# Kernel optimization log

Measured on AMD Instinct MI355X. Metric: run time of the kernel, lower is better.

Reference implementation:

```python
import jax, jax.numpy as jnp
import numpy as np

K = 1.0          # manifold curvature parameter (Lorentz hyperboloid <x,x>_L = -K)
NUM_HEADS = 16
LN_EPS = 1e-5
MID_EPS = 1e-8


def add_time(space):
    # lift a space-like vector onto the hyperboloid: x0 = sqrt(||s||^2 + K)
    t = jnp.sqrt(jnp.sum(space * space, axis=-1, keepdims=True) + K)
    return jnp.concatenate([t, space], axis=-1)


def hlinear(x, W, b):
    # Lorentz linear: dense map on full ambient vector -> space part, recompute time
    return add_time(jnp.einsum('...d,od->...o', x, W) + b)


def hyp_layernorm(x, g, b):
    s = x[..., 1:]
    mu = jnp.mean(s, axis=-1, keepdims=True)
    var = jnp.mean((s - mu) ** 2, axis=-1, keepdims=True)
    s = (s - mu) * jax.lax.rsqrt(var + LN_EPS) * g + b
    return add_time(s)


def hyp_relu(x):
    return add_time(jax.nn.relu(x[..., 1:]))


def lorentz_norm(v):
    # sqrt(|<v,v>_L|) with clamp for numerical safety
    inner = -v[..., 0] ** 2 + jnp.sum(v[..., 1:] ** 2, axis=-1)
    return jnp.sqrt(jnp.maximum(jnp.abs(inner), MID_EPS))


def midpoint_pair(z, x):
    # manifold.midpoint(stack([z, x], dim=-2)).squeeze(): mean then project back
    ave = 0.5 * (z + x)
    return jnp.sqrt(K) * ave / lorentz_norm(ave)[..., None]


def attention(x, Wq, bq, Wk, bk, Wv, bv, Wo, bo):
    B, S, D = x.shape
    dim = D - 1
    H = NUM_HEADS
    dh = dim // H

    def split_heads(t):
        # drop time, split space into heads, re-lift each head onto hyperboloid
        s = t[..., 1:].reshape(B, S, H, dh).transpose(0, 2, 1, 3)  # [B,H,S,dh]
        return add_time(s)                                          # [B,H,S,dh+1]

    qh = split_heads(hlinear(x, Wq, bq))
    kh = split_heads(hlinear(x, Wk, bk))
    vh = split_heads(hlinear(x, Wv, bv))

    # pairwise Lorentz inner product; scores = -d_L^2 / sqrt(dh)
    inner = (jnp.einsum('bhid,bhjd->bhij', qh[..., 1:], kh[..., 1:])
             - qh[..., 0][..., :, None] * kh[..., 0][..., None, :])
    scores = (2.0 / K + 2.0 * inner) / jnp.sqrt(jnp.asarray(dh, x.dtype))
    att = jax.nn.softmax(scores, axis=-1)

    # Lorentz midpoint aggregation of values (weights sum to 1)
    ave = jnp.einsum('bhij,bhjd->bhid', att, vh)
    out = jnp.sqrt(K) * ave / lorentz_norm(ave)[..., None]  # [B,H,S,dh+1]

    # concat head space parts, re-lift, output projection
    out_space = out[..., 1:].transpose(0, 2, 1, 3).reshape(B, S, dim)
    return hlinear(add_time(out_space), Wo, bo)


def reference(x, Wq, bq, Wk, bk, Wv, bv, Wo, bo, ln1_g, ln1_b, W1, c1, W2, c2, ln2_g, ln2_b):
    z = attention(x, Wq, bq, Wk, bk, Wv, bv, Wo, bo)
    x = midpoint_pair(z, x)
    x = hyp_layernorm(x, ln1_g, ln1_b)
    h = hyp_relu(hlinear(x, W1, c1))
    z = hlinear(h, W2, c2)
    x = midpoint_pair(z, x)
    x = hyp_layernorm(x, ln2_g, ln2_b)
    return x


def setup_inputs() -> dict:
    key = jax.random.key(0)
    ks = jax.random.split(key, 12)
    B, S, dim, mlp = 4, 1024, 1024, 4096
    D = dim + 1
    sc = 0.02
    x = add_time(jax.random.normal(ks[0], (B, S, dim), dtype=jnp.float32))
    return {
        'x': x,
        'Wq': sc * jax.random.normal(ks[1], (dim, D), dtype=jnp.float32),
        'bq': jnp.zeros((dim,), jnp.float32),
        'Wk': sc * jax.random.normal(ks[2], (dim, D), dtype=jnp.float32),
        'bk': jnp.zeros((dim,), jnp.float32),
        'Wv': sc * jax.random.normal(ks[3], (dim, D), dtype=jnp.float32),
        'bv': jnp.zeros((dim,), jnp.float32),
        'Wo': sc * jax.random.normal(ks[4], (dim, D), dtype=jnp.float32),
        'bo': jnp.zeros((dim,), jnp.float32),
        'ln1_g': jnp.ones((dim,), jnp.float32),
        'ln1_b': jnp.zeros((dim,), jnp.float32),
        'W1': sc * jax.random.normal(ks[5], (mlp, D), dtype=jnp.float32),
        'c1': jnp.zeros((mlp,), jnp.float32),
        'W2': sc * jax.random.normal(ks[6], (dim, mlp + 1), dtype=jnp.float32),
        'c2': jnp.zeros((dim,), jnp.float32),
        'ln2_g': jnp.ones((dim,), jnp.float32),
        'ln2_b': jnp.zeros((dim,), jnp.float32),
    }
```

## Files before the change

### kernel.cpp

```cpp
#include <hip/hip_runtime.h>

typedef unsigned short u16;
typedef unsigned int   u32;
typedef short bf16x8 __attribute__((ext_vector_type(8)));
typedef float f32x4  __attribute__((ext_vector_type(4)));

#define NTOK 4096
#define SEQ  1024

__device__ __forceinline__ u16 f2bf(float f){
  union { float f; u32 u; } x; x.f = f;
  u32 r = (x.u + 0x7FFFu + ((x.u >> 16) & 1u)) >> 16;
  return (u16)r;
}
__device__ __forceinline__ float bf2f(u16 u){
  union { u32 u; float f; } x; x.u = ((u32)u) << 16; return x.f;
}
__device__ __forceinline__ void gl_lds16(const void* gp, void* lp){
  __builtin_amdgcn_global_load_lds(
      (const __attribute__((address_space(1))) u32*)gp,
      (__attribute__((address_space(3))) u32*)lp, 16, 0, 0);
}

__global__ __launch_bounds__(256) void conv_x(const float* __restrict__ x,
                                              u16* __restrict__ xs, float* __restrict__ xt){
  int t = blockIdx.x * 256 + threadIdx.x;
  int tok = t >> 10, i = t & 1023;
  xs[t] = f2bf(x[(size_t)tok * 1025 + 1 + i]);
  if (i == 0) xt[tok] = x[(size_t)tok * 1025];
}

__global__ __launch_bounds__(256) void conv_w_all(
    const float* __restrict__ Wq, const float* __restrict__ Wk,
    const float* __restrict__ Wv, const float* __restrict__ Wo,
    const float* __restrict__ W1, const float* __restrict__ W2,
    u16* __restrict__ wqkv, u16* __restrict__ wo_s, u16* __restrict__ w1_s, u16* __restrict__ w2_s,
    float* __restrict__ wqkv0, float* __restrict__ wo0, float* __restrict__ w10, float* __restrict__ w20)
{
  int t = blockIdx.x * 256 + threadIdx.x;
  const int M1 = 1 << 20;
  const float* W; u16* Wb; float* w0; int shift; int idx;
  if (t < 4 * M1){
    int region = t >> 20; idx = t & (M1 - 1); shift = 10;
    if (region == 0)      { W = Wq; Wb = wqkv;          w0 = wqkv0; }
    else if (region == 1) { W = Wk; Wb = wqkv + M1;     w0 = wqkv0 + 1024; }
    else if (region == 2) { W = Wv; Wb = wqkv + 2 * M1; w0 = wqkv0 + 2048; }
    else                  { W = Wo; Wb = wo_s;          w0 = wo0; }
  } else if (t < 8 * M1){
    idx = t - 4 * M1; shift = 10; W = W1; Wb = w1_s; w0 = w10;
  } else {
    idx = t - 8 * M1; shift = 12; W = W2; Wb = w2_s; w0 = w20;
  }
  int Kin = 1 << shift;
  int r = idx >> shift, i = idx & (Kin - 1);
  Wb[idx] = f2bf(W[(size_t)r * (Kin + 1) + 1 + i]);
  if (i == 0) w0[r] = W[(size_t)r * (Kin + 1)];
}

__global__ __launch_bounds__(256) void v_transpose(const u16* __restrict__ qkv,
                                                   const float* __restrict__ vtm,
                                                   u16* __restrict__ vT){
  __shared__ u16 tile[64 * 72];
  const int tid = threadIdx.x;
  const int kt = blockIdx.x, bh = blockIdx.y;
  const int b = bh >> 4, h = bh & 15;
  #pragma unroll
  for (int i = 0; i < 2; i++){
    int c = tid * 2 + i;
    int key = c >> 3, fc = c & 7;
    uint4 v = *(const uint4*)(qkv + ((size_t)(b * 1024 + kt * 64 + key)) * 3072 + 2048 + h * 64 + fc * 8);
    *(uint4*)&tile[key * 72 + fc * 8] = v;
  }
  __syncthreads();
  for (int c = tid; c < 520; c += 256){
    int vtr = c >> 3, kc = c & 7;
    union { uint4 v; u16 s[8]; } d;
    if (vtr == 0){
      #pragma unroll
      for (int j = 0; j < 8; j++) d.s[j] = f2bf(vtm[(size_t)bh * 1024 + kt * 64 + kc * 8 + j]);
    } else {
      int f = vtr - 1;
      #pragma unroll
      for (int j = 0; j < 8; j++) d.s[j] = tile[(kc * 8 + j) * 72 + f];
    }
    *(uint4*)(vT + ((size_t)bh * 65 + vtr) * 1024 + kt * 64 + kc * 8) = d.v;
  }
}

__global__ __launch_bounds__(256) void gemm_bt(
    const u16* __restrict__ A, int lda, const u16* __restrict__ Bm, int ldb,
    const float* __restrict__ at, int at_mode, const float* __restrict__ b0,
    const float* __restrict__ bias_a, const float* __restrict__ bias_b, const float* __restrict__ bias_c,
    u16* __restrict__ Cbf, int ldc, int Kslice, int mode,
    float* __restrict__ qtv, float* __restrict__ ktv, float* __restrict__ vtm,
    float* __restrict__ rowsq)
{
  __shared__ u16 As[2][128 * 32];
  __shared__ u16 Bs[2][128 * 32];
  const int tid = threadIdx.x;
  const int w = tid >> 6, l = tid & 63;
  const int l15 = l & 15, q = l >> 4;
  const int m0 = blockIdx.y * 128, n0 = blockIdx.x * 128;
  const int ks = blockIdx.z;
  const int kbeg = ks * Kslice;
  const int kend = kbeg + Kslice;
  const int wr = w >> 1, wc = w & 1;
  f32x4 acc[4][4] = {};

  auto stage = [&](int kt, int buf){
    #pragma unroll
    for (int i = 0; i < 2; i++){
      int s = (w * 2 + i) * 64 + l;
      int row = s >> 2;
      int kc = ((s & 3) - (s >> 3)) & 3;
      gl_lds16(A  + (size_t)(m0 + row) * lda + kt + kc * 8,
               &As[buf][(w * 2 + i) * 512]);
      gl_lds16(Bm + (size_t)(n0 + row) * ldb + kt + kc * 8,
               &Bs[buf][(w * 2 + i) * 512]);
    }
  };
  auto compute = [&](int buf){
    bf16x8 af[4], bfr[4];
    #pragma unroll
    for (int i = 0; i < 4; i++){
      int row = wr * 64 + i * 16 + l15;
      int slot = row * 4 + ((q + (row >> 1)) & 3);
      af[i] = *(const bf16x8*)&As[buf][slot * 8];
    }
    #pragma unroll
    for (int j = 0; j < 4; j++){
      int row = wc * 64 + j * 16 + l15;
      int slot = row * 4 + ((q + (row >> 1)) & 3);
      bfr[j] = *(const bf16x8*)&Bs[buf][slot * 8];
    }
    #pragma unroll
    for (int i = 0; i < 4; i++)
      #pragma unroll
      for (int j = 0; j < 4; j++)
        acc[i][j] = __builtin_amdgcn_mfma_f32_16x16x32_bf16(af[i], bfr[j], acc[i][j], 0, 0, 0);
  };

  stage(kbeg, 0);
  for (int kt = kbeg; kt < kend; kt += 64){
    __syncthreads();
    stage(kt + 32, 1);
    compute(0);
    __syncthreads();
    if (kt + 64 < kend) stage(kt + 64, 0);
    compute(1);
  }

  const size_t slice_off = (size_t)ks * (size_t)(gridDim.y * 128) * ldc;
  #pragma unroll
  for (int i = 0; i < 4; i++){
    float atv[4];
    #pragma unroll
    for (int r = 0; r < 4; r++){
      float a = at[m0 + wr * 64 + i * 16 + q * 4 + r];
      atv[r] = at_mode ? sqrtf(a + 1.f) : a;
    }
    float p[4] = {0.f, 0.f, 0.f, 0.f};
    #pragma unroll
    for (int j = 0; j < 4; j++){
      int col = n0 + wc * 64 + j * 16 + l15;
      float b0v = b0[col];
      float bv;
      if (mode == 0) bv = (col < 1024) ? bias_a[col] : (col < 2048) ? bias_b[col - 1024] : bias_c[col - 2048];
      else bv = bias_a[col];
      #pragma unroll
      for (int r = 0; r < 4; r++){
        size_t row = (size_t)(m0 + wr * 64 + i * 16 + q * 4 + r);
        float add = (ks == 0) ? (atv[r] * b0v + bv) : 0.f;
        float v = acc[i][j][r] + add;
        if (mode == 2) v = fmaxf(v, 0.f);
        Cbf[slice_off + row * ldc + col] = f2bf(v);
        if (mode != 1) p[r] += v * v;
      }
    }
    if (mode != 1){
      #pragma unroll
      for (int r = 0; r < 4; r++){
        float s = p[r];
        s += __shfl_xor(s, 1, 64); s += __shfl_xor(s, 2, 64);
        s += __shfl_xor(s, 4, 64); s += __shfl_xor(s, 8, 64);
        if (l15 == 0){
          int row = m0 + wr * 64 + i * 16 + q * 4 + r;
          if (mode == 2){
            atomicAdd(&rowsq[row], s);
          } else {
            int ch = (n0 + wc * 64) >> 6;
            int bb = row >> 10, sidx = row & 1023;
            float t = sqrtf(s + 1.f);
            if (ch < 16)      qtv[((size_t)bb * 16 + ch) * 1024 + sidx] = t;
            else if (ch < 32) ktv[((size_t)bb * 16 + ch - 16) * 1024 + sidx] = t;
            else              vtm[((size_t)bb * 16 + ch - 32) * 1024 + sidx] = t;
          }
        }
      }
    }
  }
}

__global__ __launch_bounds__(512) void attn_kernel(
    const u16* __restrict__ qkv, const float* __restrict__ qt,
    const float* __restrict__ ktm, const u16* __restrict__ vT,
    u16* __restrict__ aout, float* __restrict__ aot_sq)
{
  __shared__ u16 smem[30720];
  u16* Qlds = smem;
  u16* Kl0 = smem + 8192;
  u16* Kl1 = smem + 12288;
  u16* Vl0 = smem + 16384;
  u16* Vl1 = smem;
  u16* Plds = smem + 21504;
  const int tid = threadIdx.x;
  const int w = tid >> 6, l = tid & 63;
  const int l15 = l & 15, qd = l >> 4;
  const int q0 = blockIdx.x * 128;
  const int bh = blockIdx.y;
  const int b = bh >> 4, h = bh & 15;
  const size_t tokbase = (size_t)b << 10;

  #pragma unroll
  for (int i = 0; i < 2; i++){
    int c = i * 512 + w * 64 + l;
    int row = c >> 3, kc = ((c & 7) - row) & 7;
    gl_lds16(qkv + (tokbase + q0 + row) * 3072 + h * 64 + kc * 8, &Qlds[(i * 512 + w * 64) * 8]);
  }
  __syncthreads();
  bf16x8 aq[2];
  {
    int row = w * 16 + l15;
    #pragma unroll
    for (int kk = 0; kk < 2; kk++)
      aq[kk] = *(const bf16x8*)&Qlds[(row * 8 + ((kk * 4 + qd + row) & 7)) * 8];
  }
  float tq[4];
  #pragma unroll
  for (int r = 0; r < 4; r++)
    tq[r] = qt[(size_t)bh * SEQ + q0 + w * 16 + qd * 4 + r];

  auto stage_kv = [&](int kt, int buf){
    u16* K = buf ? Kl1 : Kl0;
    u16* V = buf ? Vl1 : Vl0;
    int c = w * 64 + l;
    int row = c >> 3, kc = ((c & 7) - row) & 7;
    gl_lds16(qkv + (tokbase + kt * 64 + row) * 3072 + 1024 + h * 64 + kc * 8, &K[w * 512]);
    gl_lds16(vT + ((size_t)bh * 65 + row) * 1024 + kt * 64 + kc * 8, &V[w * 512]);
    if (w == 0 && l < 8)
      gl_lds16(vT + ((size_t)bh * 65 + 64) * 1024 + kt * 64 + (l & 7) * 8, &V[4096]);
  };

  float mrow[4] = {-1e30f, -1e30f, -1e30f, -1e30f};
  f32x4 acco[5] = {};

  stage_kv(0, 0);
  for (int kt = 0; kt < 16; kt++){
    __syncthreads();
    if (kt + 1 < 16) stage_kv(kt + 1, (kt + 1) & 1);
    u16* K = (kt & 1) ? Kl1 : Kl0;
    u16* V = (kt & 1) ? Vl1 : Vl0;

    float sc[4][4];
    float mx[4] = {-1e30f, -1e30f, -1e30f, -1e30f};
    #pragma unroll
    for (int ct = 0; ct < 4; ct++){
      f32x4 z = {0.f, 0.f, 0.f, 0.f};
      int key = ct * 16 + l15;
      #pragma unroll
      for (int kk = 0; kk < 2; kk++){
        bf16x8 bk = *(const bf16x8*)&K[(key * 8 + ((kk * 4 + qd + key) & 7)) * 8];
        z = __builtin_amdgcn_mfma_f32_16x16x32_bf16(aq[kk], bk, z, 0, 0, 0);
      }
      float tk = ktm[(size_t)bh * SEQ + kt * 64 + key];
      #pragma unroll
      for (int r = 0; r < 4; r++){
        float s = 0.25f + 0.25f * (z[r] - tq[r] * tk);
        sc[ct][r] = s;
        mx[r] = fmaxf(mx[r], s);
      }
    }
    #pragma unroll
    for (int r = 0; r < 4; r++){
      #pragma unroll
      for (int msk = 1; msk < 16; msk <<= 1)
        mx[r] = fmaxf(mx[r], __shfl_xor(mx[r], msk, 64));
      float mnew = fmaxf(mrow[r], mx[r]);
      float alpha = __expf(mrow[r] - mnew);
      mrow[r] = mnew;
      #pragma unroll
      for (int co = 0; co < 5; co++) acco[co][r] *= alpha;
      mx[r] = mnew;
    }
    #pragma unroll
    for (int ct = 0; ct < 4; ct++)
      #pragma unroll
      for (int r = 0; r < 4; r++)
        Plds[w * 1152 + (qd * 4 + r) * 72 + ct * 16 + l15] = f2bf(__expf(sc[ct][r] - mx[r]));
    asm volatile("s_waitcnt lgkmcnt(0)" ::: "memory");
    bf16x8 ap[2];
    #pragma unroll
    for (int kk = 0; kk < 2; kk++)
      ap[kk] = *(const bf16x8*)&Plds[w * 1152 + l15 * 72 + kk * 32 + qd * 8];
    #pragma unroll
    for (int co = 0; co < 5; co++){
      int vtr = co * 16 + l15;
      #pragma unroll
      for (int kk = 0; kk < 2; kk++){
        bf16x8 bv = *(const bf16x8*)&V[(vtr * 8 + ((kk * 4 + qd + vtr) & 7)) * 8];
        acco[co] = __builtin_amdgcn_mfma_f32_16x16x32_bf16(ap[kk], bv, acco[co], 0, 0, 0);
      }
    }
  }
  #pragma unroll
  for (int r = 0; r < 4; r++){
    float ss = 0.f;
    #pragma unroll
    for (int co = 0; co < 5; co++){
      int col = co * 16 + l15;
      float v = acco[co][r];
      if (col == 0) ss -= v * v;
      else if (col < 65) ss += v * v;
    }
    #pragma unroll
    for (int msk = 1; msk < 16; msk <<= 1) ss += __shfl_xor(ss, msk, 64);
    float v0b = __shfl(acco[0][r], l & 48, 64);
    float sp = ss + v0b * v0b;
    float rn = rsqrtf(fmaxf(fabsf(ss), 1e-8f));
    size_t rowg = tokbase + q0 + w * 16 + qd * 4 + r;
    if (l15 == 0) atomicAdd(&aot_sq[rowg], sp * rn * rn);
    #pragma unroll
    for (int co = 0; co < 5; co++){
      int col = co * 16 + l15;
      if (col >= 1 && col < 65)
        aout[rowg * 1024 + h * 64 + col - 1] = f2bf(acco[co][r] * rn);
    }
  }
}

__device__ __forceinline__ float block_sum(float v, float* red){
  int tid = threadIdx.x;
  #pragma unroll
  for (int m = 1; m < 64; m <<= 1) v += __shfl_xor(v, m, 64);
  __syncthreads();
  if ((tid & 63) == 0) red[tid >> 6] = v;
  __syncthreads();
  return red[0] + red[1] + red[2] + red[3];
}

__global__ __launch_bounds__(256) void mid_ln(
    const u16* __restrict__ z, const u16* __restrict__ xsb, const float* __restrict__ xtv,
    const float* __restrict__ gam, const float* __restrict__ bet,
    u16* __restrict__ ob, float* __restrict__ ot,
    float* __restrict__ ofull, int mode_out, int nsl)
{
  __shared__ float red[4];
  const int tid = threadIdx.x;
  const int tok = blockIdx.x;
  float zv[4], xv[4], xtime;
  xtime = xtv[tok];
  {
    const u16* xr = xsb + (size_t)tok * 1024;
    #pragma unroll
    for (int j = 0; j < 4; j++) xv[j] = bf2f(xr[tid + j * 256]);
  }
  {
    #pragma unroll
    for (int j = 0; j < 4; j++) zv[j] = 0.f;
    for (int s = 0; s < nsl; s++){
      const u16* zs = z + (size_t)s * NTOK * 1024 + (size_t)tok * 1024;
      #pragma unroll
      for (int j = 0; j < 4; j++) zv[j] += bf2f(zs[tid + j * 256]);
    }
  }
  float ssz = 0.f;
  #pragma unroll
  for (int j = 0; j < 4; j++) ssz += zv[j] * zv[j];
  ssz = block_sum(ssz, red);
  float tz = sqrtf(ssz + 1.f);
  float av[4]; float ssa = 0.f;
  #pragma unroll
  for (int j = 0; j < 4; j++){ av[j] = 0.5f * (zv[j] + xv[j]); ssa += av[j] * av[j]; }
  ssa = block_sum(ssa, red);
  float avt = 0.5f * (tz + xtime);
  float rn = rsqrtf(fmaxf(fabsf(ssa - avt * avt), 1e-8f));
  float uv[4]; float su = 0.f, squ = 0.f;
  #pragma unroll
  for (int j = 0; j < 4; j++){ uv[j] = av[j] * rn; su += uv[j]; squ += uv[j] * uv[j]; }
  su = block_sum(su, red);
  squ = block_sum(squ, red);
  float mu = su * (1.f / 1024.f);
  float var = squ * (1.f / 1024.f) - mu * mu;
  float rv = rsqrtf(fmaxf(var, 0.f) + 1e-5f);
  float sv[4]; float sss = 0.f;
  #pragma unroll
  for (int j = 0; j < 4; j++){
    int i = tid + j * 256;
    sv[j] = (uv[j] - mu) * rv * gam[i] + bet[i];
    sss += sv[j] * sv[j];
  }
  sss = block_sum(sss, red);
  float tout = sqrtf(sss + 1.f);
  if (mode_out == 0){
    #pragma unroll
    for (int j = 0; j < 4; j++){
      int i = tid + j * 256;
      ob[(size_t)tok * 1024 + i] = f2bf(sv[j]);
    }
    if (tid == 0) ot[tok] = tout;
  } else {
    float* orow = ofull + (size_t)tok * 1025;
    #pragma unroll
    for (int j = 0; j < 4; j++) orow[1 + tid + j * 256] = sv[j];
    if (tid == 0) orow[0] = tout;
  }
}

extern "C" void kernel_launch(void* const* d_in, const int* in_sizes, int n_in,
                              void* d_out, int out_size, void* d_ws, size_t ws_size,
                              hipStream_t stream){
  const float* x   = (const float*)d_in[0];
  const float* Wq  = (const float*)d_in[1];
  const float* bq  = (const float*)d_in[2];
  const float* Wk  = (const float*)d_in[3];
  const float* bk  = (const float*)d_in[4];
  const float* Wv  = (const float*)d_in[5];
  const float* bv  = (const float*)d_in[6];
  const float* Wo  = (const float*)d_in[7];
  const float* bo  = (const float*)d_in[8];
  const float* g1  = (const float*)d_in[9];
  const float* be1 = (const float*)d_in[10];
  const float* W1  = (const float*)d_in[11];
  const float* c1  = (const float*)d_in[12];
  const float* W2  = (const float*)d_in[13];
  const float* c2  = (const float*)d_in[14];
  const float* g2  = (const float*)d_in[15];
  const float* be2 = (const float*)d_in[16];
  float* out = (float*)d_out;

  char* p = (char*)d_ws;
  auto take = [&](size_t n){ char* r = p; p += (n + 255) & ~(size_t)255; return r; };
  u16*   xs    = (u16*)  take((size_t)NTOK * 1024 * 2);
  float* xt    = (float*)take(NTOK * 4);
  u16*   wqkv  = (u16*)  take((size_t)3072 * 1024 * 2);
  float* wqkv0 = (float*)take(3072 * 4);
  u16*   wo_s  = (u16*)  take((size_t)1024 * 1024 * 2);
  float* wo0   = (float*)take(1024 * 4);
  u16*   w1_s  = (u16*)  take((size_t)4096 * 1024 * 2);
  float* w10   = (float*)take(4096 * 4);
  u16*   w2_s  = (u16*)  take((size_t)1024 * 4096 * 2);
  float* w20   = (float*)take(1024 * 4);
  u16*   qkvb  = (u16*)  take((size_t)NTOK * 3072 * 2);
  float* qtv   = (float*)take((size_t)64 * 1024 * 4);
  float* ktv   = (float*)take((size_t)64 * 1024 * 4);
  float* vtm   = (float*)take((size_t)64 * 1024 * 4);
  u16*   vT    = (u16*)  take((size_t)64 * 65 * 1024 * 2);
  u16*   aoutb = (u16*)  take((size_t)NTOK * 1024 * 2);
  float* sqbuf = (float*)take((size_t)2 * NTOK * 4);
  float* aot_sq = sqbuf;
  float* htv_sq = sqbuf + NTOK;
  u16*   zbuf  = (u16*)  take((size_t)4 * NTOK * 1024 * 2);
  u16*   x1b   = (u16*)  take((size_t)NTOK * 1024 * 2);
  float* x1t   = (float*)take(NTOK * 4);
  u16*   hbuf  = (u16*)  take((size_t)NTOK * 4096 * 2);

  hipMemsetAsync(sqbuf, 0, (size_t)2 * NTOK * 4, stream);

  conv_x<<<NTOK * 1024 / 256, 256, 0, stream>>>(x, xs, xt);
  conv_w_all<<<(12 * 1024 * 1024) / 256, 256, 0, stream>>>(
      Wq, Wk, Wv, Wo, W1, W2, wqkv, wo_s, w1_s, w2_s, wqkv0, wo0, w10, w20);

  gemm_bt<<<dim3(24, 32), 256, 0, stream>>>(xs, 1024, wqkv, 1024, xt, 0, wqkv0,
      bq, bk, bv, qkvb, 3072, 1024, 0, qtv, ktv, vtm, nullptr);
  v_transpose<<<dim3(16, 64), 256, 0, stream>>>(qkvb, vtm, vT);
  attn_kernel<<<dim3(8, 64), 512, 0, stream>>>(qkvb, qtv, ktv, vT, aoutb, aot_sq);
  gemm_bt<<<dim3(8, 32, 2), 256, 0, stream>>>(aoutb, 1024, wo_s, 1024, aot_sq, 1, wo0,
      bo, nullptr, nullptr, zbuf, 1024, 512, 1, nullptr, nullptr, nullptr, nullptr);
  mid_ln<<<NTOK, 256, 0, stream>>>(zbuf, xs, xt, g1, be1,
      x1b, x1t, nullptr, 0, 2);
  gemm_bt<<<dim3(32, 32), 256, 0, stream>>>(x1b, 1024, w1_s, 1024, x1t, 0, w10,
      c1, nullptr, nullptr, hbuf, 4096, 1024, 2, nullptr, nullptr, nullptr, htv_sq);
  gemm_bt<<<dim3(8, 32, 4), 256, 0, stream>>>(hbuf, 4096, w2_s, 4096, htv_sq, 1, w20,
      c2, nullptr, nullptr, zbuf, 1024, 1024, 1, nullptr, nullptr, nullptr, nullptr);
  mid_ln<<<NTOK, 256, 0, stream>>>(zbuf, x1b, x1t, g2, be2,
      nullptr, nullptr, out, 1, 4);
}
```

Measured before the change: 467.9 us.

## Rewrite GEMM main loop with register-staged prefetch, tile swizzle, and deeper split-K

Replaces the direct global-to-LDS loads in gemm_bt with global loads into registers that are written to LDS one step later, giving a two-deep prefetch pipeline. Raw s_barrier and waitcnt instructions are issued between sched_barrier fences, and MFMA issue priority is raised. Workgroups are swizzled so that neighbouring blocks share input tiles in cache. The output projection moves from 2-way to 4-way split-K, with the matching mid_ln reduction count updated. This adds register pressure, and the hand-placed barriers could hurt if the compiler's own scheduling was already better.

Result: slower. 728.3 us (+55.7%).

```diff
diff --git a/kernel.cpp b/kernel.cpp
--- a/kernel.cpp
+++ b/kernel.cpp
@@ -7,6 +7,8 @@
 
 #define NTOK 4096
 #define SEQ  1024
+
+#define SCHEDW() __builtin_amdgcn_sched_barrier(0)
 
 __device__ __forceinline__ u16 f2bf(float f){
   union { float f; u32 u; } x; x.f = f;
@@ -88,69 +90,92 @@
 }
 
 __global__ __launch_bounds__(256) void gemm_bt(
-    const u16* __restrict__ A, int lda, const u16* __restrict__ Bm, int ldb,
+    const u16* __restrict__ Ag, int lda, const u16* __restrict__ Bg, int ldb,
     const float* __restrict__ at, int at_mode, const float* __restrict__ b0,
     const float* __restrict__ bias_a, const float* __restrict__ bias_b, const float* __restrict__ bias_c,
     u16* __restrict__ Cbf, int ldc, int Kslice, int mode,
     float* __restrict__ qtv, float* __restrict__ ktv, float* __restrict__ vtm,
     float* __restrict__ rowsq)
 {
-  __shared__ u16 As[2][128 * 32];
-  __shared__ u16 Bs[2][128 * 32];
+  __shared__ u16 A0[4096], A1[4096], B0[4096], B1[4096];
   const int tid = threadIdx.x;
   const int w = tid >> 6, l = tid & 63;
   const int l15 = l & 15, q = l >> 4;
-  const int m0 = blockIdx.y * 128, n0 = blockIdx.x * 128;
+  const int wr = w >> 1, wc = w & 1;
+  const int gx = gridDim.x;
+  const int nwg = gx * gridDim.y;
+  const int lin = blockIdx.y * gx + blockIdx.x;
+  const int swz = (lin & 7) * (nwg >> 3) + (lin >> 3);
+  const int m0 = (swz / gx) * 128, n0 = (swz % gx) * 128;
   const int ks = blockIdx.z;
   const int kbeg = ks * Kslice;
-  const int kend = kbeg + Kslice;
-  const int wr = w >> 1, wc = w & 1;
+  const int NT = Kslice >> 5;
+
   f32x4 acc[4][4] = {};
-
-  auto stage = [&](int kt, int buf){
-    #pragma unroll
-    for (int i = 0; i < 2; i++){
-      int s = (w * 2 + i) * 64 + l;
-      int row = s >> 2;
-      int kc = ((s & 3) - (s >> 3)) & 3;
-      gl_lds16(A  + (size_t)(m0 + row) * lda + kt + kc * 8,
-               &As[buf][(w * 2 + i) * 512]);
-      gl_lds16(Bm + (size_t)(n0 + row) * ldb + kt + kc * 8,
-               &Bs[buf][(w * 2 + i) * 512]);
-    }
+  uint4 ra[2], rb[2];
+
+  const int urow0 = tid >> 2, uc0 = tid & 3;
+  const int urow1 = (tid + 256) >> 2, uc1 = tid & 3;
+  const int slotA0 = urow0 * 4 + ((uc0 + (urow0 >> 1)) & 3);
+  const int slotA1 = urow1 * 4 + ((uc1 + (urow1 >> 1)) & 3);
+
+  auto gload = [&](int kt){
+    ra[0] = *(const uint4*)(Ag + (size_t)(m0 + urow0) * lda + kt + uc0 * 8);
+    ra[1] = *(const uint4*)(Ag + (size_t)(m0 + urow1) * lda + kt + uc1 * 8);
+    rb[0] = *(const uint4*)(Bg + (size_t)(n0 + urow0) * ldb + kt + uc0 * 8);
+    rb[1] = *(const uint4*)(Bg + (size_t)(n0 + urow1) * ldb + kt + uc1 * 8);
   };
-  auto compute = [&](int buf){
+  auto swrite = [&](u16* Ad, u16* Bd){
+    *(uint4*)&Ad[slotA0 * 8] = ra[0];
+    *(uint4*)&Ad[slotA1 * 8] = ra[1];
+    *(uint4*)&Bd[slotA0 * 8] = rb[0];
+    *(uint4*)&Bd[slotA1 * 8] = rb[1];
+  };
+  auto phase = [&](const u16* Ad, const u16* Bd){
     bf16x8 af[4], bfr[4];
     #pragma unroll
     for (int i = 0; i < 4; i++){
       int row = wr * 64 + i * 16 + l15;
       int slot = row * 4 + ((q + (row >> 1)) & 3);
-      af[i] = *(const bf16x8*)&As[buf][slot * 8];
+      af[i] = *(const bf16x8*)&Ad[slot * 8];
     }
     #pragma unroll
     for (int j = 0; j < 4; j++){
       int row = wc * 64 + j * 16 + l15;
       int slot = row * 4 + ((q + (row >> 1)) & 3);
-      bfr[j] = *(const bf16x8*)&Bs[buf][slot * 8];
-    }
+      bfr[j] = *(const bf16x8*)&Bd[slot * 8];
+    }
+    __builtin_amdgcn_s_setprio(1);
     #pragma unroll
     for (int i = 0; i < 4; i++)
       #pragma unroll
       for (int j = 0; j < 4; j++)
         acc[i][j] = __builtin_amdgcn_mfma_f32_16x16x32_bf16(af[i], bfr[j], acc[i][j], 0, 0, 0);
+    __builtin_amdgcn_s_setprio(0);
   };
 
-  stage(kbeg, 0);
-  for (int kt = kbeg; kt < kend; kt += 64){
-    __syncthreads();
-    stage(kt + 32, 1);
-    compute(0);
-    __syncthreads();
-    if (kt + 64 < kend) stage(kt + 64, 0);
-    compute(1);
-  }
-
-  const size_t slice_off = (size_t)ks * (size_t)(gridDim.y * 128) * ldc;
+  gload(kbeg);
+  swrite(A0, B0);
+  if (NT > 1) gload(kbeg + 32);
+
+  for (int U = 0; U < NT; U++){
+    u16* Awr = (U & 1) ? A0 : A1;
+    u16* Bwr = (U & 1) ? B0 : B1;
+    const u16* Ard = (U & 1) ? A1 : A0;
+    const u16* Brd = (U & 1) ? B1 : B0;
+    if (U + 1 < NT) swrite(Awr, Bwr);
+    if (U + 2 < NT) gload(kbeg + (U + 2) * 32);
+    SCHEDW();
+    asm volatile("s_waitcnt lgkmcnt(0)\n\ts_barrier" ::: "memory");
+    SCHEDW();
+    phase(Ard, Brd);
+    SCHEDW();
+    asm volatile("s_barrier" ::: "memory");
+    SCHEDW();
+  }
+
+  const size_t Mtot = (size_t)gridDim.y * 128;
+  const size_t slice_off = (size_t)ks * Mtot * ldc;
   #pragma unroll
   for (int i = 0; i < 4; i++){
     float atv[4];
@@ -474,10 +499,10 @@
       bq, bk, bv, qkvb, 3072, 1024, 0, qtv, ktv, vtm, nullptr);
   v_transpose<<<dim3(16, 64), 256, 0, stream>>>(qkvb, vtm, vT);
   attn_kernel<<<dim3(8, 64), 512, 0, stream>>>(qkvb, qtv, ktv, vT, aoutb, aot_sq);
-  gemm_bt<<<dim3(8, 32, 2), 256, 0, stream>>>(aoutb, 1024, wo_s, 1024, aot_sq, 1, wo0,
-      bo, nullptr, nullptr, zbuf, 1024, 512, 1, nullptr, nullptr, nullptr, nullptr);
+  gemm_bt<<<dim3(8, 32, 4), 256, 0, stream>>>(aoutb, 1024, wo_s, 1024, aot_sq, 1, wo0,
+      bo, nullptr, nullptr, zbuf, 1024, 256, 1, nullptr, nullptr, nullptr, nullptr);
   mid_ln<<<NTOK, 256, 0, stream>>>(zbuf, xs, xt, g1, be1,
-      x1b, x1t, nullptr, 0, 2);
+      x1b, x1t, nullptr, 0, 4);
   gemm_bt<<<dim3(32, 32), 256, 0, stream>>>(x1b, 1024, w1_s, 1024, x1t, 0, w10,
       c1, nullptr, nullptr, hbuf, 4096, 1024, 2, nullptr, nullptr, nullptr, htv_sq);
   gemm_bt<<<dim3(8, 32, 4), 256, 0, stream>>>(hbuf, 4096, w2_s, 4096, htv_sq, 1, w20,
```
